# Kernel optimization log

Hardware: AMD Instinct MI355X
Metric: run time of the kernel (lower is better)

The kernel has to match this reference:

```python
import jax, jax.numpy as jnp
import numpy as np

B, N, D = 32, 4096, 256
NC, NTPC, NVPT, NS = 16, 8, 4, 16
NT = NC * NTPC          # 128 type codes
NV = NT * NVPT          # 512 variant codes
THRESH = 0.1            # code_sparsity


def setup_inputs() -> dict:
    key = jax.random.key(0)
    ks = jax.random.split(key, 24)
    rn = lambda k, s, sc=0.02: jax.random.normal(k, s, jnp.float32) * sc
    return {
        "X": jax.random.normal(ks[0], (B, N, D), jnp.float32),
        "positions": jax.random.normal(ks[1], (B, N, D), jnp.float32),
        "mask": jnp.ones((B, N), jnp.bool_),
        "category_codes": rn(ks[2], (NC, D)),
        "type_codes": rn(ks[3], (NT, D)),
        "variant_codes": rn(ks[4], (NV, D)),
        "spatial_codes": rn(ks[5], (NS, D)),
        "log_tau": jnp.zeros((1,), jnp.float32),
        "Wk": rn(ks[6], (D, D)), "bk": jnp.zeros((D,), jnp.float32),
        "Wcat": rn(ks[7], (D, D)), "bcat": jnp.zeros((D,), jnp.float32),
        "Wtype": rn(ks[8], (D, D)), "btype": jnp.zeros((D,), jnp.float32),
        "Wvar": rn(ks[9], (D, D)), "bvar": jnp.zeros((D,), jnp.float32),
        "Wsp": rn(ks[10], (D, D)), "bsp": jnp.zeros((D,), jnp.float32),
        "Wg1": rn(ks[11], (D, 2 * D)), "bg1": jnp.zeros((D,), jnp.float32),
        "Wg2": rn(ks[12], (D, D)), "bg2": jnp.zeros((D,), jnp.float32),
        "Wo": rn(ks[13], (D, D)), "bo": jnp.zeros((D,), jnp.float32),
        "ln_g": jnp.ones((D,), jnp.float32), "ln_b": jnp.zeros((D,), jnp.float32),
        "level_weights": jnp.ones((4,), jnp.float32) / 4.0,
    }


def _sparsify(w, thr):
    w = jnp.where(w > thr, w, 0.0)
    return w / (w.sum(-1, keepdims=True) + 1e-8)


def reference(X, positions, mask, category_codes, type_codes, variant_codes,
              spatial_codes, log_tau, Wk, bk, Wcat, bcat, Wtype, btype,
              Wvar, bvar, Wsp, bsp, Wg1, bg1, Wg2, bg2, Wo, bo, ln_g, ln_b,
              level_weights):
    d = X.shape[-1]
    tau = jnp.clip(jnp.exp(log_tau) + 0.1, 0.1, 2.0)  # (1,)
    mv = jnp.finfo(X.dtype).min / 2
    K = X @ Wk.T + bk  # (B,N,d)

    def level(codes, Wq, bq):
        Q = codes @ Wq.T + bq                                    # (M,d)
        attn = jnp.einsum('md,bnd->bmn', Q, K) / jnp.sqrt(jnp.float32(d))
        attn = jnp.where(mask[:, None, :], attn, mv)
        attn = jnp.clip(attn, -50.0, 50.0)
        G = jnp.nan_to_num(jax.nn.softmax(attn, axis=-1))
        H = jnp.einsum('bmn,bnd->bmd', G, X)                     # (B,M,d)
        w_raw = jnp.linalg.norm(H, axis=-1) / tau                # (B,M)
        return H, w_raw

    # level 0: category
    H_cat, w_cat_raw = level(category_codes, Wcat, bcat)
    w_cat_sparse = _sparsify(jax.nn.softmax(w_cat_raw, -1), THRESH)
    # level 1: type (gated by category)
    H_type, w_type_raw = level(type_codes, Wtype, btype)
    w_type_g = (w_type_raw.reshape(-1, NC, NTPC) * w_cat_sparse[:, :, None]).reshape(-1, NT)
    w_type_sparse = _sparsify(jax.nn.softmax(w_type_g, -1), THRESH / 2)
    # level 2: variant (gated by type)
    H_var, w_var_raw = level(variant_codes, Wvar, bvar)
    w_type_exp = jnp.repeat(w_type_sparse, NVPT, axis=-1)        # (B,NV)
    w_var_sparse = _sparsify(jax.nn.softmax(w_var_raw * w_type_exp, -1), THRESH / 4)
    # spatial (independent)
    H_sp, w_sp_raw = level(spatial_codes, Wsp, bsp)
    w_sp_sparse = _sparsify(jax.nn.softmax(w_sp_raw, -1), THRESH)

    z_cat = jnp.einsum('bm,bmd->bd', w_cat_sparse, H_cat)
    z_type = jnp.einsum('bm,bmd->bd', w_type_sparse, H_type)
    z_var = jnp.einsum('bm,bmd->bd', w_var_sparse, H_var)
    z_sp = jnp.einsum('bm,bmd->bd', w_sp_sparse, H_sp)

    lw = jax.nn.softmax(level_weights)
    z = lw[0] * z_cat + lw[1] * z_type + lw[2] * z_var + lw[3] * z_sp

    # position gate: masked mean-pooled positions -> sigmoid gate
    m = mask.astype(X.dtype)
    pos_pool = (positions * m[:, :, None]).sum(1) / (m.sum(1, keepdims=True) + 1e-8)
    h = jax.nn.gelu(jnp.concatenate([z, pos_pool], -1) @ Wg1.T + bg1, approximate=False)
    gate = jax.nn.sigmoid(h @ Wg2.T + bg2)
    z = z * gate

    # out_proj: Linear + LayerNorm
    y = z @ Wo.T + bo
    mu = y.mean(-1, keepdims=True)
    var = ((y - mu) ** 2).mean(-1, keepdims=True)
    y = (y - mu) / jnp.sqrt(var + 1e-5) * ln_g + ln_b
    return y
```

## Files before the change

kernel.cpp:

```cpp
#include <hip/hip_runtime.h>

typedef unsigned short u16;
typedef short v8s __attribute__((ext_vector_type(8)));
typedef float v4f __attribute__((ext_vector_type(4)));

union U16x8 { uint4 u4; v8s s8; u16 us[8]; };

__device__ __forceinline__ u16 f2bf(float x) {
  unsigned int u = __float_as_uint(x);
  u += 0x7fffu + ((u >> 16) & 1u);
  return (u16)(u >> 16);
}

#define GLOBAL_AS __attribute__((address_space(1)))
#define LDS_AS __attribute__((address_space(3)))
__device__ __forceinline__ void async16(const void* g, void* l) {
  __builtin_amdgcn_global_load_lds((const GLOBAL_AS unsigned int*)g,
                                   (LDS_AS unsigned int*)l, 16, 0, 0);
}

#define BB 32
#define NN 4096
#define DD 256
#define M_TOT 672
#define M_PAD 704

__global__ void kz_zero(float* __restrict__ p, int n) {
  int i = blockIdx.x * 256 + threadIdx.x;
  if (i < n) p[i] = 0.f;
}

__global__ void k0_q(const float* __restrict__ cat, const float* __restrict__ typ,
                     const float* __restrict__ var, const float* __restrict__ spc,
                     const float* __restrict__ Wcat, const float* __restrict__ bcat,
                     const float* __restrict__ Wtype, const float* __restrict__ btype,
                     const float* __restrict__ Wvar, const float* __restrict__ bvar,
                     const float* __restrict__ Wsp, const float* __restrict__ bsp,
                     float* __restrict__ Qall) {
  __shared__ float cl[DD];
  const int m = blockIdx.x, tid = threadIdx.x;
  const float* codes = nullptr; const float* W = nullptr; const float* bia = nullptr; int r = 0;
  if (m < 16)       { codes = cat; r = m;       W = Wcat;  bia = bcat; }
  else if (m < 144) { codes = typ; r = m - 16;  W = Wtype; bia = btype; }
  else if (m < 656) { codes = var; r = m - 144; W = Wvar;  bia = bvar; }
  else if (m < 672) { codes = spc; r = m - 656; W = Wsp;   bia = bsp; }
  cl[tid] = (m < M_TOT) ? codes[r * DD + tid] : 0.f;
  __syncthreads();
  if (m < M_TOT) {
    float acc = bia[tid];
    const float4* w4 = (const float4*)(W + (size_t)tid * DD);
    const float4* c4 = (const float4*)cl;
    #pragma unroll 8
    for (int k = 0; k < 64; ++k) {
      float4 a = c4[k], b = w4[k];
      acc += a.x * b.x + a.y * b.y + a.z * b.z + a.w * b.w;
    }
    Qall[m * DD + tid] = acc;
  } else {
    Qall[m * DD + tid] = 0.f;
  }
}

__global__ void k1_qp(const float* __restrict__ Qall, const float* __restrict__ Wk,
                      const float* __restrict__ bk, u16* __restrict__ Qp,
                      float* __restrict__ qbw) {
  __shared__ float ql[DD];
  __shared__ float red[4];
  const int m = blockIdx.x, tid = threadIdx.x;
  ql[tid] = Qall[m * DD + tid];
  __syncthreads();
  float acc = 0.f;
  for (int j = 0; j < DD; ++j) acc += ql[j] * Wk[(size_t)j * DD + tid];
  Qp[m * DD + tid] = f2bf(acc);
  float p = ql[tid] * bk[tid];
  #pragma unroll
  for (int off = 32; off > 0; off >>= 1) p += __shfl_down(p, off, 64);
  if ((tid & 63) == 0) red[tid >> 6] = p;
  __syncthreads();
  if (tid == 0) qbw[m] = red[0] + red[1] + red[2] + red[3];
}

__global__ void k2_cast(const float* __restrict__ X, u16* __restrict__ Xb,
                        u16* __restrict__ XbT) {
  __shared__ u16 tl[64][72];
  const int n0 = blockIdx.x * 64, d0 = blockIdx.y * 64, b = blockIdx.z;
  const int tid = threadIdx.x;
  const int nl = tid >> 4, d4 = tid & 15;
  #pragma unroll
  for (int rr = 0; rr < 4; ++rr) {
    const int n = n0 + nl + rr * 16;
    float4 v = *(const float4*)(X + ((size_t)b * NN + n) * DD + d0 + d4 * 4);
    ushort4 h;
    h.x = f2bf(v.x); h.y = f2bf(v.y); h.z = f2bf(v.z); h.w = f2bf(v.w);
    *(ushort4*)(Xb + ((size_t)b * NN + n) * DD + d0 + d4 * 4) = h;
    *(ushort4*)(&tl[nl + rr * 16][d4 * 4]) = h;
  }
  __syncthreads();
  const int dl = tid >> 4, n4 = tid & 15;
  #pragma unroll
  for (int rr = 0; rr < 4; ++rr) {
    const int d = dl + rr * 16;
    ushort4 h;
    h.x = tl[n4 * 4 + 0][d]; h.y = tl[n4 * 4 + 1][d];
    h.z = tl[n4 * 4 + 2][d]; h.w = tl[n4 * 4 + 3][d];
    *(ushort4*)(XbT + ((size_t)b * DD + d0 + d) * NN + n0 + n4 * 4) = h;
  }
}

__global__ __launch_bounds__(256, 2) void p1_scores(
    const u16* __restrict__ Xb, const u16* __restrict__ Qp,
    const float* __restrict__ qbw, const unsigned char* __restrict__ mask,
    u16* __restrict__ P, float* __restrict__ sums, int b0) {
  __shared__ u16 sA[128 * 64];
  __shared__ u16 sB[128 * 64];
  const int tid = threadIdx.x;
  const int lane = tid & 63, w = tid >> 6;
  const int q = lane >> 4, c16 = lane & 15;
  const int n0 = blockIdx.x * 128, m0 = blockIdx.y * 128;
  const int b = b0 + blockIdx.z;
  const int wm = (w >> 1) * 64, wn = (w & 1) * 64;

  float qv[4][4];
  unsigned char mk[4];
  #pragma unroll
  for (int mi = 0; mi < 4; ++mi)
    #pragma unroll
    for (int r = 0; r < 4; ++r) {
      int row = m0 + wm + mi * 16 + q * 4 + r;
      qv[mi][r] = qbw[row < M_PAD ? row : M_PAD - 1];
    }
  #pragma unroll
  for (int ni = 0; ni < 4; ++ni)
    mk[ni] = mask[(size_t)b * NN + n0 + wn + ni * 16 + c16];

  v4f acc[4][4];
  #pragma unroll
  for (int mi = 0; mi < 4; ++mi)
    #pragma unroll
    for (int ni = 0; ni < 4; ++ni) acc[mi][ni] = (v4f){0.f, 0.f, 0.f, 0.f};

  const u16* Xbase = Xb + (size_t)b * NN * DD;
  for (int ks = 0; ks < 4; ++ks) {
    __syncthreads();
    #pragma unroll
    for (int i = 0; i < 4; ++i) {
      const int c = i * 256 + tid;
      const int row = c >> 3, kc = (c & 7) * 8;
      int gm = m0 + row; gm = gm < M_PAD ? gm : M_PAD - 1;
      async16(Qp + (size_t)gm * DD + ks * 64 + kc, sA + c * 8);
      async16(Xbase + (size_t)(n0 + row) * DD + ks * 64 + kc, sB + c * 8);
    }
    __syncthreads();
    #pragma unroll
    for (int kk = 0; kk < 2; ++kk) {
      v8s af[4], bf[4];
      #pragma unroll
      for (int mi = 0; mi < 4; ++mi) {
        U16x8 u; u.u4 = *(const uint4*)(sA + (wm + mi * 16 + c16) * 64 + kk * 32 + q * 8);
        af[mi] = u.s8;
      }
      #pragma unroll
      for (int ni = 0; ni < 4; ++ni) {
        U16x8 u; u.u4 = *(const uint4*)(sB + (wn + ni * 16 + c16) * 64 + kk * 32 + q * 8);
        bf[ni] = u.s8;
      }
      #pragma unroll
      for (int mi = 0; mi < 4; ++mi)
        #pragma unroll
        for (int ni = 0; ni < 4; ++ni)
          acc[mi][ni] = __builtin_amdgcn_mfma_f32_16x16x32_bf16(af[mi], bf[ni], acc[mi][ni], 0, 0, 0);
    }
  }

  float rs[4][4];
  #pragma unroll
  for (int mi = 0; mi < 4; ++mi)
    #pragma unroll
    for (int r = 0; r < 4; ++r) rs[mi][r] = 0.f;

  #pragma unroll
  for (int mi = 0; mi < 4; ++mi) {
    #pragma unroll
    for (int ni = 0; ni < 4; ++ni) {
      #pragma unroll
      for (int r = 0; r < 4; ++r) {
        float s = (acc[mi][ni][r] + qv[mi][r]) * 0.0625f;
        s = fminf(fmaxf(s, -50.f), 50.f);
        s = mk[ni] ? s : -50.f;
        float p = __expf(s);
        rs[mi][r] += p;
        const int row = m0 + wm + mi * 16 + q * 4 + r;
        if (row < M_TOT)
          P[((size_t)(b - b0) * M_TOT + row) * NN + n0 + wn + ni * 16 + c16] = f2bf(p);
      }
    }
  }
  #pragma unroll
  for (int mi = 0; mi < 4; ++mi) {
    #pragma unroll
    for (int r = 0; r < 4; ++r) {
      float v = rs[mi][r];
      v += __shfl_xor(v, 1, 64);
      v += __shfl_xor(v, 2, 64);
      v += __shfl_xor(v, 4, 64);
      v += __shfl_xor(v, 8, 64);
      const int row = m0 + wm + mi * 16 + q * 4 + r;
      if (c16 == 0 && row < M_TOT)
        atomicAdd(&sums[(size_t)b * M_PAD + row], v);
    }
  }
}

__global__ __launch_bounds__(256, 4) void p2_h(
    const u16* __restrict__ P, const u16* __restrict__ XbT,
    const float* __restrict__ sums, float* __restrict__ Hws,
    float* __restrict__ nrm, int b0) {
  __shared__ u16 sA[64 * 64];
  __shared__ u16 sB[128 * 64];
  const int tid = threadIdx.x;
  const int lane = tid & 63, w = tid >> 6;
  const int q = lane >> 4, c16 = lane & 15;
  const int d0 = blockIdx.x * 128, m0 = blockIdx.y * 64;
  const int b = b0 + blockIdx.z;
  const int wm = (w >> 1) * 32, wd = (w & 1) * 64;

  v4f acc[2][4];
  #pragma unroll
  for (int mi = 0; mi < 2; ++mi)
    #pragma unroll
    for (int ni = 0; ni < 4; ++ni) acc[mi][ni] = (v4f){0.f, 0.f, 0.f, 0.f};

  const u16* Pb = P + (size_t)(b - b0) * M_TOT * NN;
  const u16* Tb = XbT + ((size_t)b * DD + d0) * NN;

  for (int ks = 0; ks < NN / 64; ++ks) {
    __syncthreads();
    #pragma unroll
    for (int i = 0; i < 2; ++i) {
      const int c = i * 256 + tid;
      const int row = c >> 3, kc = (c & 7) * 8;
      int gm = m0 + row; gm = gm < M_TOT ? gm : M_TOT - 1;
      async16(Pb + (size_t)gm * NN + ks * 64 + kc, sA + c * 8);
    }
    #pragma unroll
    for (int i = 0; i < 4; ++i) {
      const int c = i * 256 + tid;
      const int row = c >> 3, kc = (c & 7) * 8;
      async16(Tb + (size_t)row * NN + ks * 64 + kc, sB + c * 8);
    }
    __syncthreads();
    #pragma unroll
    for (int kk = 0; kk < 2; ++kk) {
      v8s af[2], bf[4];
      #pragma unroll
      for (int mi = 0; mi < 2; ++mi) {
        U16x8 u; u.u4 = *(const uint4*)(sA + (wm + mi * 16 + c16) * 64 + kk * 32 + q * 8);
        af[mi] = u.s8;
      }
      #pragma unroll
      for (int ni = 0; ni < 4; ++ni) {
        U16x8 u; u.u4 = *(const uint4*)(sB + (wd + ni * 16 + c16) * 64 + kk * 32 + q * 8);
        bf[ni] = u.s8;
      }
      #pragma unroll
      for (int mi = 0; mi < 2; ++mi)
        #pragma unroll
        for (int ni = 0; ni < 4; ++ni)
          acc[mi][ni] = __builtin_amdgcn_mfma_f32_16x16x32_bf16(af[mi], bf[ni], acc[mi][ni], 0, 0, 0);
    }
  }

  float sv[2][4], ns[2][4];
  #pragma unroll
  for (int mi = 0; mi < 2; ++mi)
    #pragma unroll
    for (int r = 0; r < 4; ++r) {
      const int row = m0 + wm + mi * 16 + q * 4 + r;
      sv[mi][r] = sums[(size_t)b * M_PAD + row];
      ns[mi][r] = 0.f;
    }
  #pragma unroll
  for (int mi = 0; mi < 2; ++mi) {
    #pragma unroll
    for (int ni = 0; ni < 4; ++ni) {
      #pragma unroll
      for (int r = 0; r < 4; ++r) {
        const int row = m0 + wm + mi * 16 + q * 4 + r;
        float h = acc[mi][ni][r] / sv[mi][r];
        ns[mi][r] += h * h;
        Hws[((size_t)b * M_PAD + row) * DD + d0 + wd + ni * 16 + c16] = h;
      }
    }
  }
  #pragma unroll
  for (int mi = 0; mi < 2; ++mi) {
    #pragma unroll
    for (int r = 0; r < 4; ++r) {
      float v = ns[mi][r];
      v += __shfl_xor(v, 1, 64);
      v += __shfl_xor(v, 2, 64);
      v += __shfl_xor(v, 4, 64);
      v += __shfl_xor(v, 8, 64);
      const int row = m0 + wm + mi * 16 + q * 4 + r;
      if (c16 == 0 && row < M_TOT)
        atomicAdd(&nrm[(size_t)b * M_PAD + row], v);
    }
  }
}

__global__ void k4_pool(const float* __restrict__ pos, const unsigned char* __restrict__ mask,
                        float* __restrict__ pp, float* __restrict__ cnt) {
  __shared__ float sp[4][256];
  __shared__ float sc[4];
  const int cx = blockIdx.x, b = blockIdx.y, tid = threadIdx.x;
  const int nl = tid >> 6, d4 = tid & 63;
  const int n0 = cx * 256;
  float4 acc = {0.f, 0.f, 0.f, 0.f};
  float c = 0.f;
  for (int i = 0; i < 64; ++i) {
    const int n = n0 + i * 4 + nl;
    const float m = mask[(size_t)b * NN + n] ? 1.f : 0.f;
    c += m;
    float4 v = *(const float4*)(pos + ((size_t)b * NN + n) * DD + d4 * 4);
    acc.x += m * v.x; acc.y += m * v.y; acc.z += m * v.z; acc.w += m * v.w;
  }
  *(float4*)(&sp[nl][d4 * 4]) = acc;
  if (d4 == 0) sc[nl] = c;
  __syncthreads();
  pp[((size_t)b * 16 + cx) * DD + tid] = sp[0][tid] + sp[1][tid] + sp[2][tid] + sp[3][tid];
  if (tid == 0) cnt[b * 16 + cx] = sc[0] + sc[1] + sc[2] + sc[3];
}

__device__ void softmax_sparsify(const float* in, int nn, float* outp, float thr) {
  float mx = -3.4e38f;
  for (int i = 0; i < nn; ++i) mx = fmaxf(mx, in[i]);
  float s = 0.f;
  for (int i = 0; i < nn; ++i) { float e = __expf(in[i] - mx); outp[i] = e; s += e; }
  float s2 = 0.f;
  for (int i = 0; i < nn; ++i) {
    float v = outp[i] / s;
    v = (v > thr) ? v : 0.f;
    outp[i] = v; s2 += v;
  }
  const float inv = 1.f / (s2 + 1e-8f);
  for (int i = 0; i < nn; ++i) outp[i] *= inv;
}

__global__ void k5a_weights(const float* __restrict__ nrm, const float* __restrict__ log_tau,
                            const float* __restrict__ lvlw, float* __restrict__ wbufG) {
  __shared__ float wr[M_TOT];
  __shared__ float wcat[16], wtyp[128], wvar[512], wsp[16], lw[4];
  __shared__ float tmp[128];
  const int b = blockIdx.x, tid = threadIdx.x;
  const float tau = fminf(fmaxf(__expf(log_tau[0]) + 0.1f, 0.1f), 2.0f);
  for (int m = tid; m < M_TOT; m += 256)
    wr[m] = sqrtf(nrm[(size_t)b * M_PAD + m]) / tau;
  __syncthreads();
  if (tid == 0) {
    softmax_sparsify(wr, 16, wcat, 0.1f);
    for (int i = 0; i < 128; ++i) tmp[i] = wr[16 + i] * wcat[i >> 3];
    softmax_sparsify(tmp, 128, wtyp, 0.05f);
    for (int i = 0; i < 512; ++i) wvar[i] = wr[144 + i] * wtyp[i >> 2];
    softmax_sparsify(wvar, 512, wvar, 0.025f);
    softmax_sparsify(wr + 656, 16, wsp, 0.1f);
    float mx = fmaxf(fmaxf(lvlw[0], lvlw[1]), fmaxf(lvlw[2], lvlw[3]));
    float s = 0.f;
    for (int i = 0; i < 4; ++i) { lw[i] = __expf(lvlw[i] - mx); s += lw[i]; }
    for (int i = 0; i < 4; ++i) lw[i] /= s;
  }
  __syncthreads();
  for (int m = tid; m < M_TOT; m += 256) {
    float v;
    if (m < 16)       v = lw[0] * wcat[m];
    else if (m < 144) v = lw[1] * wtyp[m - 16];
    else if (m < 656) v = lw[2] * wvar[m - 144];
    else              v = lw[3] * wsp[m - 656];
    wbufG[(size_t)b * M_PAD + m] = v;
  }
}

__global__ void k5b_z(const float* __restrict__ Hws, const float* __restrict__ wbufG,
                      float* __restrict__ zacc) {
  const int mc = blockIdx.x, b = blockIdx.y, tid = threadIdx.x;
  const float* Hb = Hws + (size_t)b * M_PAD * DD;
  const float* wb = wbufG + (size_t)b * M_PAD;
  float acc = 0.f;
  #pragma unroll 4
  for (int i = 0; i < 84; ++i) {
    const int m = mc * 84 + i;
    acc += wb[m] * Hb[(size_t)m * DD + tid];
  }
  atomicAdd(&zacc[(size_t)b * DD + tid], acc);
}

__global__ void k5c_mlp(const float* __restrict__ zacc, const float* __restrict__ pp,
                        const float* __restrict__ cnt,
                        const float* __restrict__ Wg1, const float* __restrict__ bg1,
                        const float* __restrict__ Wg2, const float* __restrict__ bg2,
                        const float* __restrict__ Wo, const float* __restrict__ bo,
                        const float* __restrict__ lng, const float* __restrict__ lnb,
                        float* __restrict__ out) {
  __shared__ float zb[DD], pb[DD], hb[DD], zg[DD];
  __shared__ float red[8];
  const int b = blockIdx.x, tid = threadIdx.x;
  const int lane = tid & 63, w = tid >> 6;

  float p = 0.f, c = 0.f;
  for (int ch = 0; ch < 16; ++ch) {
    p += pp[((size_t)b * 16 + ch) * DD + tid];
    c += cnt[b * 16 + ch];
  }
  zb[tid] = zacc[(size_t)b * DD + tid];
  pb[tid] = p / (c + 1e-8f);
  __syncthreads();

  float h = bg1[tid];
  {
    const float4* w4 = (const float4*)(Wg1 + (size_t)tid * 512);
    const float4* z4 = (const float4*)zb;
    const float4* p4 = (const float4*)pb;
    for (int k = 0; k < 64; ++k) {
      float4 a = z4[k], bb = w4[k];
      h += a.x * bb.x + a.y * bb.y + a.z * bb.z + a.w * bb.w;
    }
    for (int k = 0; k < 64; ++k) {
      float4 a = p4[k], bb = w4[64 + k];
      h += a.x * bb.x + a.y * bb.y + a.z * bb.z + a.w * bb.w;
    }
  }
  h = 0.5f * h * (1.f + erff(h * 0.70710678118654752f));
  hb[tid] = h;
  __syncthreads();

  float g = bg2[tid];
  {
    const float4* w4 = (const float4*)(Wg2 + (size_t)tid * DD);
    const float4* h4 = (const float4*)hb;
    for (int k = 0; k < 64; ++k) {
      float4 a = h4[k], bb = w4[k];
      g += a.x * bb.x + a.y * bb.y + a.z * bb.z + a.w * bb.w;
    }
  }
  g = 1.f / (1.f + __expf(-g));
  zg[tid] = zb[tid] * g;
  __syncthreads();

  float y = bo[tid];
  {
    const float4* w4 = (const float4*)(Wo + (size_t)tid * DD);
    const float4* z4 = (const float4*)zg;
    for (int k = 0; k < 64; ++k) {
      float4 a = z4[k], bb = w4[k];
      y += a.x * bb.x + a.y * bb.y + a.z * bb.z + a.w * bb.w;
    }
  }

  float s = y;
  #pragma unroll
  for (int off = 32; off > 0; off >>= 1) s += __shfl_xor(s, off, 64);
  if (lane == 0) red[w] = s;
  __syncthreads();
  const float mu = (red[0] + red[1] + red[2] + red[3]) * (1.f / 256.f);
  float dv = (y - mu) * (y - mu);
  #pragma unroll
  for (int off = 32; off > 0; off >>= 1) dv += __shfl_xor(dv, off, 64);
  if (lane == 0) red[4 + w] = dv;
  __syncthreads();
  const float var = (red[4] + red[5] + red[6] + red[7]) * (1.f / 256.f);
  out[(size_t)b * DD + tid] = (y - mu) / sqrtf(var + 1e-5f) * lng[tid] + lnb[tid];
}

extern "C" void kernel_launch(void* const* d_in, const int* in_sizes, int n_in,
                              void* d_out, int out_size, void* d_ws, size_t ws_size,
                              hipStream_t stream) {
  const float* X          = (const float*)d_in[0];
  const float* positions  = (const float*)d_in[1];
  const unsigned char* mask = (const unsigned char*)d_in[2];
  const float* cat  = (const float*)d_in[3];
  const float* typ  = (const float*)d_in[4];
  const float* var  = (const float*)d_in[5];
  const float* spc  = (const float*)d_in[6];
  const float* log_tau = (const float*)d_in[7];
  const float* Wk   = (const float*)d_in[8];   const float* bk    = (const float*)d_in[9];
  const float* Wcat = (const float*)d_in[10];  const float* bcat  = (const float*)d_in[11];
  const float* Wtype= (const float*)d_in[12];  const float* btype = (const float*)d_in[13];
  const float* Wvar = (const float*)d_in[14];  const float* bvar  = (const float*)d_in[15];
  const float* Wsp  = (const float*)d_in[16];  const float* bsp   = (const float*)d_in[17];
  const float* Wg1  = (const float*)d_in[18];  const float* bg1   = (const float*)d_in[19];
  const float* Wg2  = (const float*)d_in[20];  const float* bg2   = (const float*)d_in[21];
  const float* Wo   = (const float*)d_in[22];  const float* bo    = (const float*)d_in[23];
  const float* lng  = (const float*)d_in[24];  const float* lnb   = (const float*)d_in[25];
  const float* lvlw = (const float*)d_in[26];

  char* ws = (char*)d_ws;
  size_t off = 0;
  auto alloc = [&](size_t bytes) { size_t o = off; off = (off + bytes + 255) & ~255ULL; return o; };
  const size_t oXb   = alloc((size_t)BB * NN * DD * 2);
  const size_t oXT   = alloc((size_t)BB * DD * NN * 2);
  const size_t oQall = alloc((size_t)M_PAD * DD * 4);
  const size_t oQp   = alloc((size_t)M_PAD * DD * 2);
  const size_t oQb   = alloc((size_t)M_PAD * 4);
  const size_t oSums = alloc((size_t)BB * M_PAD * 4);
  const size_t oNrm  = alloc((size_t)BB * M_PAD * 4);
  const size_t oZac  = alloc((size_t)BB * DD * 4);
  const size_t oWbf  = alloc((size_t)BB * M_PAD * 4);
  const size_t oH    = alloc((size_t)BB * M_PAD * DD * 4);
  const size_t oPP   = alloc((size_t)BB * 16 * DD * 4);
  const size_t oCNT  = alloc((size_t)BB * 16 * 4);
  const size_t oP    = alloc(0);

  const size_t pFull = (size_t)BB * M_TOT * NN * 2;
  const int chunks  = (ws_size >= oP + pFull) ? 1 : 2;
  const int chunkB  = BB / chunks;

  u16*   Xb   = (u16*)(ws + oXb);
  u16*   XbT  = (u16*)(ws + oXT);
  float* Qall = (float*)(ws + oQall);
  u16*   Qp   = (u16*)(ws + oQp);
  float* qbw  = (float*)(ws + oQb);
  float* sums = (float*)(ws + oSums);
  float* nrm  = (float*)(ws + oNrm);
  float* zacc = (float*)(ws + oZac);
  float* wbfG = (float*)(ws + oWbf);
  float* Hws  = (float*)(ws + oH);
  float* ppw  = (float*)(ws + oPP);
  float* cntw = (float*)(ws + oCNT);
  u16*   P    = (u16*)(ws + oP);

  const int nzero = 2 * BB * M_PAD + BB * DD;
  kz_zero<<<(nzero + 255) / 256, 256, 0, stream>>>(sums, nzero);
  k0_q<<<M_PAD, 256, 0, stream>>>(cat, typ, var, spc, Wcat, bcat, Wtype, btype,
                                  Wvar, bvar, Wsp, bsp, Qall);
  k1_qp<<<M_PAD, 256, 0, stream>>>(Qall, Wk, bk, Qp, qbw);
  k2_cast<<<dim3(64, 4, 32), 256, 0, stream>>>(X, Xb, XbT);
  k4_pool<<<dim3(16, 32), 256, 0, stream>>>(positions, mask, ppw, cntw);
  for (int chunk = 0; chunk < chunks; ++chunk) {
    const int b0 = chunk * chunkB;
    p1_scores<<<dim3(32, 6, chunkB), 256, 0, stream>>>(Xb, Qp, qbw, mask, P, sums, b0);
    p2_h<<<dim3(2, 11, chunkB), 256, 0, stream>>>(P, XbT, sums, Hws, nrm, b0);
  }
  k5a_weights<<<32, 256, 0, stream>>>(nrm, log_tau, lvlw, wbfG);
  k5b_z<<<dim3(8, 32), 256, 0, stream>>>(Hws, wbfG, zacc);
  k5c_mlp<<<32, 256, 0, stream>>>(zacc, ppw, cntw, Wg1, bg1, Wg2, bg2, Wo, bo,
                                  lng, lnb, (float*)d_out);
}
```

Before: 745.5 us.

## Fuse score and aggregation GEMMs into one flash-style kernel with swizzled LDS

Replaces the two-pass design, which wrote a bf16 probability matrix P to global memory and read it back, with a single fused kernel. Each block holds 64 code rows for one batch, streams N in 64-column tiles, computes exp scores into LDS and immediately accumulates P·X^T into registers. Row sums and norms are now written once per block instead of through atomics, and the normalisation by the row sum moves into k5a_weights. X and X^T are stored with XOR-swizzled columns to avoid LDS bank conflicts. The cost is that each block reloads the full X tile per batch, which is 11x redundant across code tiles, and only 352 blocks run with large LDS use per block.

```diff
diff --git a/kernel.cpp b/kernel.cpp
--- a/kernel.cpp
+++ b/kernel.cpp
@@ -24,6 +24,7 @@
 #define DD 256
 #define M_TOT 672
 #define M_PAD 704
+#define MT_PER_B 11
 
 __global__ void kz_zero(float* __restrict__ p, int n) {
   int i = blockIdx.x * 256 + threadIdx.x;
@@ -92,7 +93,8 @@
     float4 v = *(const float4*)(X + ((size_t)b * NN + n) * DD + d0 + d4 * 4);
     ushort4 h;
     h.x = f2bf(v.x); h.y = f2bf(v.y); h.z = f2bf(v.z); h.w = f2bf(v.w);
-    *(ushort4*)(Xb + ((size_t)b * NN + n) * DD + d0 + d4 * 4) = h;
+    *(ushort4*)(Xb + ((size_t)b * NN + n) * DD + d0 +
+                (((d4 >> 1) ^ (n & 7)) << 3) + (d4 & 1) * 4) = h;
     *(ushort4*)(&tl[nl + rr * 16][d4 * 4]) = h;
   }
   __syncthreads();
@@ -103,100 +105,161 @@
     ushort4 h;
     h.x = tl[n4 * 4 + 0][d]; h.y = tl[n4 * 4 + 1][d];
     h.z = tl[n4 * 4 + 2][d]; h.w = tl[n4 * 4 + 3][d];
-    *(ushort4*)(XbT + ((size_t)b * DD + d0 + d) * NN + n0 + n4 * 4) = h;
-  }
-}
-
-__global__ __launch_bounds__(256, 2) void p1_scores(
-    const u16* __restrict__ Xb, const u16* __restrict__ Qp,
-    const float* __restrict__ qbw, const unsigned char* __restrict__ mask,
-    u16* __restrict__ P, float* __restrict__ sums, int b0) {
-  __shared__ u16 sA[128 * 64];
-  __shared__ u16 sB[128 * 64];
+    *(ushort4*)(XbT + ((size_t)b * DD + d0 + d) * NN + n0 +
+                (((n4 >> 1) ^ (dl & 7)) << 3) + (n4 & 1) * 4) = h;
+  }
+}
+
+__global__ __launch_bounds__(256, 2) void pf_fused(
+    const u16* __restrict__ Xb, const u16* __restrict__ XbT,
+    const u16* __restrict__ Qp, const float* __restrict__ qbw,
+    const unsigned char* __restrict__ mask,
+    float* __restrict__ Hws, float* __restrict__ sums, float* __restrict__ nrm) {
+  __shared__ u16 sX[64 * 256];
+  __shared__ u16 sXT[256 * 64];
+  __shared__ u16 sP[64 * 64];
+
+  const int id = blockIdx.x;
+  const int orig = (id & 7) * 44 + (id >> 3);
+  const int b = orig / MT_PER_B;
+  const int m0 = (orig - b * MT_PER_B) * 64;
+
   const int tid = threadIdx.x;
   const int lane = tid & 63, w = tid >> 6;
   const int q = lane >> 4, c16 = lane & 15;
-  const int n0 = blockIdx.x * 128, m0 = blockIdx.y * 128;
-  const int b = b0 + blockIdx.z;
-  const int wm = (w >> 1) * 64, wn = (w & 1) * 64;
-
-  float qv[4][4];
-  unsigned char mk[4];
+  const int wmQ = (w >> 1) * 32, wn = (w & 1) * 32;
+  const int wd = w * 64;
+
+  v8s aq[2][4][2];
+  #pragma unroll
+  for (int mi = 0; mi < 2; ++mi) {
+    const u16* qrow = Qp + (size_t)(m0 + wmQ + mi * 16 + c16) * DD;
+    #pragma unroll
+    for (int ks = 0; ks < 4; ++ks)
+      #pragma unroll
+      for (int kk = 0; kk < 2; ++kk) {
+        U16x8 u; u.u4 = *(const uint4*)(qrow + ks * 64 + kk * 32 + q * 8);
+        aq[mi][ks][kk] = u.s8;
+      }
+  }
+  float qv[2][4];
+  #pragma unroll
+  for (int mi = 0; mi < 2; ++mi)
+    #pragma unroll
+    for (int r = 0; r < 4; ++r)
+      qv[mi][r] = qbw[m0 + wmQ + mi * 16 + q * 4 + r];
+
+  v4f hacc[4][4];
   #pragma unroll
   for (int mi = 0; mi < 4; ++mi)
     #pragma unroll
-    for (int r = 0; r < 4; ++r) {
-      int row = m0 + wm + mi * 16 + q * 4 + r;
-      qv[mi][r] = qbw[row < M_PAD ? row : M_PAD - 1];
-    }
-  #pragma unroll
-  for (int ni = 0; ni < 4; ++ni)
-    mk[ni] = mask[(size_t)b * NN + n0 + wn + ni * 16 + c16];
-
-  v4f acc[4][4];
+    for (int di = 0; di < 4; ++di) hacc[mi][di] = (v4f){0.f, 0.f, 0.f, 0.f};
+  float rs[2][4];
+  #pragma unroll
+  for (int mi = 0; mi < 2; ++mi)
+    #pragma unroll
+    for (int r = 0; r < 4; ++r) rs[mi][r] = 0.f;
+
+  const u16* XbB = Xb + (size_t)b * NN * DD;
+  const u16* XTB = XbT + (size_t)b * DD * NN;
+  const unsigned char* mkB = mask + (size_t)b * NN;
+
+  for (int it = 0; it < 64; ++it) {
+    const int n0g = it * 64;
+    __syncthreads();
+    #pragma unroll
+    for (int i = 0; i < 8; ++i) {
+      const int c = i * 256 + tid;
+      async16(XbB + (size_t)(n0g + (c >> 5)) * DD + (c & 31) * 8, sX + c * 8);
+    }
+    #pragma unroll
+    for (int i = 0; i < 8; ++i) {
+      const int c = i * 256 + tid;
+      async16(XTB + (size_t)(c >> 3) * NN + n0g + (c & 7) * 8, sXT + c * 8);
+    }
+    __syncthreads();
+
+    v4f sacc[2][2];
+    #pragma unroll
+    for (int mi = 0; mi < 2; ++mi)
+      #pragma unroll
+      for (int ni = 0; ni < 2; ++ni) sacc[mi][ni] = (v4f){0.f, 0.f, 0.f, 0.f};
+    #pragma unroll
+    for (int ks = 0; ks < 4; ++ks)
+      #pragma unroll
+      for (int kk = 0; kk < 2; ++kk) {
+        v8s bq[2];
+        #pragma unroll
+        for (int ni = 0; ni < 2; ++ni) {
+          const int n = wn + ni * 16 + c16;
+          U16x8 u;
+          u.u4 = *(const uint4*)(sX + n * 256 + (((ks * 8 + kk * 4 + q) ^ (n & 7)) << 3));
+          bq[ni] = u.s8;
+        }
+        #pragma unroll
+        for (int mi = 0; mi < 2; ++mi)
+          #pragma unroll
+          for (int ni = 0; ni < 2; ++ni)
+            sacc[mi][ni] = __builtin_amdgcn_mfma_f32_16x16x32_bf16(
+                aq[mi][ks][kk], bq[ni], sacc[mi][ni], 0, 0, 0);
+      }
+
+    #pragma unroll
+    for (int ni = 0; ni < 2; ++ni) {
+      const int nl = wn + ni * 16 + c16;
+      const bool mk = mkB[n0g + nl] != 0;
+      #pragma unroll
+      for (int mi = 0; mi < 2; ++mi)
+        #pragma unroll
+        for (int r = 0; r < 4; ++r) {
+          float s = (sacc[mi][ni][r] + qv[mi][r]) * 0.0625f;
+          s = fminf(fmaxf(s, -50.f), 50.f);
+          s = mk ? s : -50.f;
+          float p = __expf(s);
+          rs[mi][r] += p;
+          const int ml = wmQ + mi * 16 + q * 4 + r;
+          sP[ml * 64 + (nl ^ ((ml & 7) << 3))] = f2bf(p);
+        }
+    }
+    __syncthreads();
+
+    #pragma unroll
+    for (int kk = 0; kk < 2; ++kk) {
+      v8s pa[4];
+      #pragma unroll
+      for (int mi = 0; mi < 4; ++mi) {
+        const int ml = mi * 16 + c16;
+        U16x8 u;
+        u.u4 = *(const uint4*)(sP + ml * 64 + ((kk * 32 + q * 8) ^ ((ml & 7) << 3)));
+        pa[mi] = u.s8;
+      }
+      #pragma unroll
+      for (int di = 0; di < 4; ++di) {
+        const int d = wd + di * 16 + c16;
+        U16x8 u;
+        u.u4 = *(const uint4*)(sXT + d * 64 + (((kk * 4 + q) ^ (d & 7)) << 3));
+        #pragma unroll
+        for (int mi = 0; mi < 4; ++mi)
+          hacc[mi][di] = __builtin_amdgcn_mfma_f32_16x16x32_bf16(
+              pa[mi], u.s8, hacc[mi][di], 0, 0, 0);
+      }
+    }
+  }
+
   #pragma unroll
   for (int mi = 0; mi < 4; ++mi)
     #pragma unroll
-    for (int ni = 0; ni < 4; ++ni) acc[mi][ni] = (v4f){0.f, 0.f, 0.f, 0.f};
-
-  const u16* Xbase = Xb + (size_t)b * NN * DD;
-  for (int ks = 0; ks < 4; ++ks) {
-    __syncthreads();
-    #pragma unroll
-    for (int i = 0; i < 4; ++i) {
-      const int c = i * 256 + tid;
-      const int row = c >> 3, kc = (c & 7) * 8;
-      int gm = m0 + row; gm = gm < M_PAD ? gm : M_PAD - 1;
-      async16(Qp + (size_t)gm * DD + ks * 64 + kc, sA + c * 8);
-      async16(Xbase + (size_t)(n0 + row) * DD + ks * 64 + kc, sB + c * 8);
-    }
-    __syncthreads();
-    #pragma unroll
-    for (int kk = 0; kk < 2; ++kk) {
-      v8s af[4], bf[4];
-      #pragma unroll
-      for (int mi = 0; mi < 4; ++mi) {
-        U16x8 u; u.u4 = *(const uint4*)(sA + (wm + mi * 16 + c16) * 64 + kk * 32 + q * 8);
-        af[mi] = u.s8;
+    for (int di = 0; di < 4; ++di)
+      #pragma unroll
+      for (int r = 0; r < 4; ++r) {
+        const int m = m0 + mi * 16 + q * 4 + r;
+        Hws[((size_t)b * M_PAD + m) * DD + wd + di * 16 + c16] = hacc[mi][di][r];
       }
-      #pragma unroll
-      for (int ni = 0; ni < 4; ++ni) {
-        U16x8 u; u.u4 = *(const uint4*)(sB + (wn + ni * 16 + c16) * 64 + kk * 32 + q * 8);
-        bf[ni] = u.s8;
-      }
-      #pragma unroll
-      for (int mi = 0; mi < 4; ++mi)
-        #pragma unroll
-        for (int ni = 0; ni < 4; ++ni)
-          acc[mi][ni] = __builtin_amdgcn_mfma_f32_16x16x32_bf16(af[mi], bf[ni], acc[mi][ni], 0, 0, 0);
-    }
-  }
-
-  float rs[4][4];
-  #pragma unroll
-  for (int mi = 0; mi < 4; ++mi)
-    #pragma unroll
-    for (int r = 0; r < 4; ++r) rs[mi][r] = 0.f;
-
-  #pragma unroll
-  for (int mi = 0; mi < 4; ++mi) {
-    #pragma unroll
-    for (int ni = 0; ni < 4; ++ni) {
-      #pragma unroll
-      for (int r = 0; r < 4; ++r) {
-        float s = (acc[mi][ni][r] + qv[mi][r]) * 0.0625f;
-        s = fminf(fmaxf(s, -50.f), 50.f);
-        s = mk[ni] ? s : -50.f;
-        float p = __expf(s);
-        rs[mi][r] += p;
-        const int row = m0 + wm + mi * 16 + q * 4 + r;
-        if (row < M_TOT)
-          P[((size_t)(b - b0) * M_TOT + row) * NN + n0 + wn + ni * 16 + c16] = f2bf(p);
-      }
-    }
-  }
-  #pragma unroll
-  for (int mi = 0; mi < 4; ++mi) {
+
+  __syncthreads();
+  float* fred = (float*)sP;
+  #pragma unroll
+  for (int mi = 0; mi < 2; ++mi)
     #pragma unroll
     for (int r = 0; r < 4; ++r) {
       float v = rs[mi][r];
@@ -204,107 +267,29 @@
       v += __shfl_xor(v, 2, 64);
       v += __shfl_xor(v, 4, 64);
       v += __shfl_xor(v, 8, 64);
-      const int row = m0 + wm + mi * 16 + q * 4 + r;
-      if (c16 == 0 && row < M_TOT)
-        atomicAdd(&sums[(size_t)b * M_PAD + row], v);
-    }
-  }
-}
-
-__global__ __launch_bounds__(256, 4) void p2_h(
-    const u16* __restrict__ P, const u16* __restrict__ XbT,
-    const float* __restrict__ sums, float* __restrict__ Hws,
-    float* __restrict__ nrm, int b0) {
-  __shared__ u16 sA[64 * 64];
-  __shared__ u16 sB[128 * 64];
-  const int tid = threadIdx.x;
-  const int lane = tid & 63, w = tid >> 6;
-  const int q = lane >> 4, c16 = lane & 15;
-  const int d0 = blockIdx.x * 128, m0 = blockIdx.y * 64;
-  const int b = b0 + blockIdx.z;
-  const int wm = (w >> 1) * 32, wd = (w & 1) * 64;
-
-  v4f acc[2][4];
-  #pragma unroll
-  for (int mi = 0; mi < 2; ++mi)
-    #pragma unroll
-    for (int ni = 0; ni < 4; ++ni) acc[mi][ni] = (v4f){0.f, 0.f, 0.f, 0.f};
-
-  const u16* Pb = P + (size_t)(b - b0) * M_TOT * NN;
-  const u16* Tb = XbT + ((size_t)b * DD + d0) * NN;
-
-  for (int ks = 0; ks < NN / 64; ++ks) {
-    __syncthreads();
-    #pragma unroll
-    for (int i = 0; i < 2; ++i) {
-      const int c = i * 256 + tid;
-      const int row = c >> 3, kc = (c & 7) * 8;
-      int gm = m0 + row; gm = gm < M_TOT ? gm : M_TOT - 1;
-      async16(Pb + (size_t)gm * NN + ks * 64 + kc, sA + c * 8);
-    }
-    #pragma unroll
-    for (int i = 0; i < 4; ++i) {
-      const int c = i * 256 + tid;
-      const int row = c >> 3, kc = (c & 7) * 8;
-      async16(Tb + (size_t)row * NN + ks * 64 + kc, sB + c * 8);
-    }
-    __syncthreads();
-    #pragma unroll
-    for (int kk = 0; kk < 2; ++kk) {
-      v8s af[2], bf[4];
-      #pragma unroll
-      for (int mi = 0; mi < 2; ++mi) {
-        U16x8 u; u.u4 = *(const uint4*)(sA + (wm + mi * 16 + c16) * 64 + kk * 32 + q * 8);
-        af[mi] = u.s8;
+      if (c16 == 0) fred[(w & 1) * 64 + wmQ + mi * 16 + q * 4 + r] = v;
+    }
+  #pragma unroll
+  for (int mi = 0; mi < 4; ++mi)
+    #pragma unroll
+    for (int r = 0; r < 4; ++r) {
+      float v = 0.f;
+      #pragma unroll
+      for (int di = 0; di < 4; ++di) {
+        float h = hacc[mi][di][r];
+        v += h * h;
       }
-      #pragma unroll
-      for (int ni = 0; ni < 4; ++ni) {
-        U16x8 u; u.u4 = *(const uint4*)(sB + (wd + ni * 16 + c16) * 64 + kk * 32 + q * 8);
-        bf[ni] = u.s8;
-      }
-      #pragma unroll
-      for (int mi = 0; mi < 2; ++mi)
-        #pragma unroll
-        for (int ni = 0; ni < 4; ++ni)
-          acc[mi][ni] = __builtin_amdgcn_mfma_f32_16x16x32_bf16(af[mi], bf[ni], acc[mi][ni], 0, 0, 0);
-    }
-  }
-
-  float sv[2][4], ns[2][4];
-  #pragma unroll
-  for (int mi = 0; mi < 2; ++mi)
-    #pragma unroll
-    for (int r = 0; r < 4; ++r) {
-      const int row = m0 + wm + mi * 16 + q * 4 + r;
-      sv[mi][r] = sums[(size_t)b * M_PAD + row];
-      ns[mi][r] = 0.f;
-    }
-  #pragma unroll
-  for (int mi = 0; mi < 2; ++mi) {
-    #pragma unroll
-    for (int ni = 0; ni < 4; ++ni) {
-      #pragma unroll
-      for (int r = 0; r < 4; ++r) {
-        const int row = m0 + wm + mi * 16 + q * 4 + r;
-        float h = acc[mi][ni][r] / sv[mi][r];
-        ns[mi][r] += h * h;
-        Hws[((size_t)b * M_PAD + row) * DD + d0 + wd + ni * 16 + c16] = h;
-      }
-    }
-  }
-  #pragma unroll
-  for (int mi = 0; mi < 2; ++mi) {
-    #pragma unroll
-    for (int r = 0; r < 4; ++r) {
-      float v = ns[mi][r];
       v += __shfl_xor(v, 1, 64);
       v += __shfl_xor(v, 2, 64);
       v += __shfl_xor(v, 4, 64);
       v += __shfl_xor(v, 8, 64);
-      const int row = m0 + wm + mi * 16 + q * 4 + r;
-      if (c16 == 0 && row < M_TOT)
-        atomicAdd(&nrm[(size_t)b * M_PAD + row], v);
-    }
+      if (c16 == 0) fred[128 + w * 64 + mi * 16 + q * 4 + r] = v;
+    }
+  __syncthreads();
+  if (tid < 64) {
+    const size_t o = (size_t)b * M_PAD + m0 + tid;
+    sums[o] = fred[tid] + fred[64 + tid];
+    nrm[o] = fred[128 + tid] + fred[192 + tid] + fred[256 + tid] + fred[320 + tid];
   }
 }
 
@@ -346,7 +331,8 @@
   for (int i = 0; i < nn; ++i) outp[i] *= inv;
 }
 
-__global__ void k5a_weights(const float* __restrict__ nrm, const float* __restrict__ log_tau,
+__global__ void k5a_weights(const float* __restrict__ nrm, const float* __restrict__ sums,
+                            const float* __restrict__ log_tau,
                             const float* __restrict__ lvlw, float* __restrict__ wbufG) {
   __shared__ float wr[M_TOT];
   __shared__ float wcat[16], wtyp[128], wvar[512], wsp[16], lw[4];
@@ -354,7 +340,7 @@
   const int b = blockIdx.x, tid = threadIdx.x;
   const float tau = fminf(fmaxf(__expf(log_tau[0]) + 0.1f, 0.1f), 2.0f);
   for (int m = tid; m < M_TOT; m += 256)
-    wr[m] = sqrtf(nrm[(size_t)b * M_PAD + m]) / tau;
+    wr[m] = sqrtf(nrm[(size_t)b * M_PAD + m]) / (sums[(size_t)b * M_PAD + m] * tau);
   __syncthreads();
   if (tid == 0) {
     softmax_sparsify(wr, 16, wcat, 0.1f);
@@ -375,7 +361,7 @@
     else if (m < 144) v = lw[1] * wtyp[m - 16];
     else if (m < 656) v = lw[2] * wvar[m - 144];
     else              v = lw[3] * wsp[m - 656];
-    wbufG[(size_t)b * M_PAD + m] = v;
+    wbufG[(size_t)b * M_PAD + m] = v / sums[(size_t)b * M_PAD + m];
   }
 }
 
@@ -507,11 +493,6 @@
   const size_t oH    = alloc((size_t)BB * M_PAD * DD * 4);
   const size_t oPP   = alloc((size_t)BB * 16 * DD * 4);
   const size_t oCNT  = alloc((size_t)BB * 16 * 4);
-  const size_t oP    = alloc(0);
-
-  const size_t pFull = (size_t)BB * M_TOT * NN * 2;
-  const int chunks  = (ws_size >= oP + pFull) ? 1 : 2;
-  const int chunkB  = BB / chunks;
 
   u16*   Xb   = (u16*)(ws + oXb);
   u16*   XbT  = (u16*)(ws + oXT);
@@ -525,21 +506,17 @@
   float* Hws  = (float*)(ws + oH);
   float* ppw  = (float*)(ws + oPP);
   float* cntw = (float*)(ws + oCNT);
-  u16*   P    = (u16*)(ws + oP);
-
-  const int nzero = 2 * BB * M_PAD + BB * DD;
-  kz_zero<<<(nzero + 255) / 256, 256, 0, stream>>>(sums, nzero);
+
+  const int nzero = BB * DD;
+  kz_zero<<<(nzero + 255) / 256, 256, 0, stream>>>(zacc, nzero);
   k0_q<<<M_PAD, 256, 0, stream>>>(cat, typ, var, spc, Wcat, bcat, Wtype, btype,
                                   Wvar, bvar, Wsp, bsp, Qall);
   k1_qp<<<M_PAD, 256, 0, stream>>>(Qall, Wk, bk, Qp, qbw);
   k2_cast<<<dim3(64, 4, 32), 256, 0, stream>>>(X, Xb, XbT);
   k4_pool<<<dim3(16, 32), 256, 0, stream>>>(positions, mask, ppw, cntw);
-  for (int chunk = 0; chunk < chunks; ++chunk) {
-    const int b0 = chunk * chunkB;
-    p1_scores<<<dim3(32, 6, chunkB), 256, 0, stream>>>(Xb, Qp, qbw, mask, P, sums, b0);
-    p2_h<<<dim3(2, 11, chunkB), 256, 0, stream>>>(P, XbT, sums, Hws, nrm, b0);
-  }
-  k5a_weights<<<32, 256, 0, stream>>>(nrm, log_tau, lvlw, wbfG);
+  pf_fused<<<dim3(BB * MT_PER_B), 256, 0, stream>>>(Xb, XbT, Qp, qbw, mask,
+                                                    Hws, sums, nrm);
+  k5a_weights<<<32, 256, 0, stream>>>(nrm, sums, log_tau, lvlw, wbfG);
   k5b_z<<<dim3(8, 32), 256, 0, stream>>>(Hws, wbfG, zacc);
   k5c_mlp<<<32, 256, 0, stream>>>(zacc, ppw, cntw, Wg1, bg1, Wg2, bg2, Wo, bo,
                                   lng, lnb, (float*)d_out);
```

Measured after the change: 743.3 us. About the same (-0.3%).
